# Kernel optimization log

Measured on AMD Instinct MI355X. Metric: run time of the kernel, lower is better.

Reference implementation:

```python
import jax, jax.numpy as jnp
import numpy as np

B = 16384
NUM_RATE, NUM_GENRE, NUM_DIRECTOR, NUM_ACTOR = 6, 25, 2186, 8030
EMB = 32


def setup_inputs() -> dict:
    key = jax.random.key(0)
    k0, k1, k2, k3, k4 = jax.random.split(key, 5)
    x = jax.random.randint(k0, (B, 1 + NUM_GENRE + NUM_DIRECTOR + NUM_ACTOR), 0, 2, dtype=jnp.int64 if jax.config.jax_enable_x64 else jnp.int32)
    rate_table = jax.random.normal(k1, (NUM_RATE, EMB), dtype=jnp.float32)
    # torch Linear weights have shape [out_features, in_features]
    W_genre = jax.random.normal(k2, (EMB, NUM_GENRE), dtype=jnp.float32) * (1.0 / np.sqrt(NUM_GENRE))
    W_director = jax.random.normal(k3, (EMB, NUM_DIRECTOR), dtype=jnp.float32) * (1.0 / np.sqrt(NUM_DIRECTOR))
    W_actor = jax.random.normal(k4, (EMB, NUM_ACTOR), dtype=jnp.float32) * (1.0 / np.sqrt(NUM_ACTOR))
    return {"x": x, "rate_table": rate_table, "W_genre": W_genre,
            "W_director": W_director, "W_actor": W_actor}


def _maxnorm_gather(table, idx, max_norm=1.0, eps=1e-7):
    # torch.nn.Embedding(max_norm=1.0): rows accessed are renormalized to norm <= max_norm
    rows = table[idx]  # [B, E]
    norm = jnp.linalg.norm(rows, axis=-1, keepdims=True)
    scale = jnp.where(norm > max_norm, max_norm / (norm + eps), 1.0)
    return rows * scale


def _mean_pool_linear(multi_hot_f, W):
    # Linear(no bias) on multi-hot then divide by row-sum == mean-pooled embedding bag
    emb = jnp.einsum('bn,en->be', multi_hot_f, W)
    return emb / jnp.sum(multi_hot_f, axis=1, keepdims=True)


def reference(x, rate_table, W_genre, W_director, W_actor):
    rate_idx = x[:, 0]
    genre = x[:, 1:26].astype(jnp.float32)
    director = x[:, 26:2212].astype(jnp.float32)
    actors = x[:, 2212:10242].astype(jnp.float32)
    rate_emb = _maxnorm_gather(rate_table, rate_idx)
    genre_emb = _mean_pool_linear(genre, W_genre)
    director_emb = _mean_pool_linear(director, W_director)
    actors_emb = _mean_pool_linear(actors, W_actor)
    return jnp.concatenate((rate_emb, genre_emb, director_emb, actors_emb), axis=1)  # [B, 4*EMB]
```

## Files before the change

kernel.cpp:

```cpp
#include <hip/hip_runtime.h>
#include <hip/hip_bf16.h>

#define B_ROWS 16384
#define XC     10242
#define NGENRE 25
#define NDIR   2186
#define NACT   8030
#define EMB    32
#define KT_TOTAL 321
#define OUTC   128
#define NCOLS  112
#define PART_STRIDE ((size_t)B_ROWS * NCOLS)
#define WFRAG_BYTES ((size_t)KT_TOTAL * 4 * 64 * 16)

typedef short bf16x8 __attribute__((ext_vector_type(8)));
typedef float f32x4  __attribute__((ext_vector_type(4)));
typedef float f32x4a __attribute__((ext_vector_type(4), aligned(4)));
typedef int   i32x4a __attribute__((ext_vector_type(4), aligned(4)));

__global__ void prep_wfrag(const float* __restrict__ wg,
                           const float* __restrict__ wd,
                           const float* __restrict__ wa,
                           uint4* __restrict__ Wfrag) {
  const int kt = blockIdx.x;
  const int s  = threadIdx.x >> 6;
  const int l  = threadIdx.x & 63;
  const int n  = l & 15;
  const int k0 = kt * 32 + ((l >> 4) << 3);

  unsigned short v[8];
#pragma unroll
  for (int j = 0; j < 8; ++j) {
    const int k = k0 + j;
    float f = 0.f;
    if (kt == 0) {
      if (s < 2) { if (k >= 1 && k < 26) f = wg[(s * 16 + n) * NGENRE + (k - 1)]; }
      else       { if (k >= 26)          f = wd[((s - 2) * 16 + n) * NDIR + (k - 26)]; }
    } else if (kt < 69) {
      if (s < 2) f = wd[(s * 16 + n) * NDIR + (k - 26)];
    } else if (kt == 69) {
      if (s < 2) { if (k < 2212)  f = wd[(s * 16 + n) * NDIR + (k - 26)]; }
      else       { if (k >= 2212) f = wa[((s - 2) * 16 + n) * NACT + (k - 2212)]; }
    } else if (kt < 320) {
      if (s < 2) f = wa[(s * 16 + n) * NACT + (k - 2212)];
    } else {
      if (s < 2 && k < XC) f = wa[(s * 16 + n) * NACT + (k - 2212)];
    }
    __hip_bfloat16 h = __float2bfloat16(f);
    v[j] = *reinterpret_cast<unsigned short*>(&h);
  }
  union { unsigned short u[8]; uint4 q; } cv;
#pragma unroll
  for (int j = 0; j < 8; ++j) cv.u[j] = v[j];
  Wfrag[((size_t)kt * 4 + s) * 64 + l] = cv.q;
}

template<int KS>
__global__ __launch_bounds__(256) void main_mm(const int* __restrict__ x,
                                               const uint4* __restrict__ Wfrag,
                                               float* __restrict__ part) {
  constexpr int PER = (((KT_TOTAL + KS - 1) / KS) + 3) & ~3;
  const int t    = threadIdx.x;
  const int rb   = blockIdx.x & 255;
  const int ks   = blockIdx.x >> 8;
  const int ktA  = ks * PER;
  const int ktB  = (ktA + PER < KT_TOTAL) ? ktA + PER : KT_TOTAL;
  const int lane = t & 63;
  const int w    = t >> 6;
  const int lo   = lane & 15, hi = lane >> 4;
  const int* xrow = x + (size_t)(rb * 64 + w * 16 + lo) * XC;

  f32x4 accG0 = {0,0,0,0}, accG1 = {0,0,0,0};
  f32x4 accD0 = {0,0,0,0}, accD1 = {0,0,0,0};
  f32x4 accA0 = {0,0,0,0}, accA1 = {0,0,0,0};
  f32x4 accI  = {0,0,0,0};

  auto load_x8 = [&](int kt, int* dst) {
    int k0 = kt * 32 + hi * 8;
    if (kt < 320) {
      i32x4a a = *reinterpret_cast<const i32x4a*>(xrow + k0);
      i32x4a b = *reinterpret_cast<const i32x4a*>(xrow + k0 + 4);
      dst[0]=a[0]; dst[1]=a[1]; dst[2]=a[2]; dst[3]=a[3];
      dst[4]=b[0]; dst[5]=b[1]; dst[6]=b[2]; dst[7]=b[3];
    } else {
#pragma unroll
      for (int j = 0; j < 8; ++j) dst[j] = (k0 + j < XC) ? xrow[k0 + j] : 0;
    }
  };
  auto packa = [&](const int* cx) -> bf16x8 {
    union { unsigned int w4[4]; bf16x8 v; } af;
#pragma unroll
    for (int i = 0; i < 4; ++i)
      af.w4[i] = ((unsigned)cx[2*i] + ((unsigned)cx[2*i+1] << 16)) * 0x3F80u;
    return af.v;
  };
  auto bload = [&](int kt, int s) -> bf16x8 {
    union { uint4 q; bf16x8 v; } c;
    c.q = Wfrag[((size_t)kt * 4 + s) * 64 + lane];
    return c.v;
  };
  auto mkconst = [&](bool on) -> bf16x8 {
    union { unsigned int w4[4]; bf16x8 v; } c;
    unsigned int u = on ? 0x3F803F80u : 0u;
    c.w4[0]=u; c.w4[1]=u; c.w4[2]=u; c.w4[3]=u;
    return c.v;
  };
  const bf16x8 ivD = mkconst(lo == 1);
  const bf16x8 ivA = mkconst(lo == 2);

  auto do_mfma = [&](int kt, bf16x8 a) {
    const int kb = kt * 32 + hi * 8;
    if (kt == 0) {
      accG0 = __builtin_amdgcn_mfma_f32_16x16x32_bf16(a, bload(0,0), accG0, 0,0,0);
      accG1 = __builtin_amdgcn_mfma_f32_16x16x32_bf16(a, bload(0,1), accG1, 0,0,0);
      accD0 = __builtin_amdgcn_mfma_f32_16x16x32_bf16(a, bload(0,2), accD0, 0,0,0);
      accD1 = __builtin_amdgcn_mfma_f32_16x16x32_bf16(a, bload(0,3), accD1, 0,0,0);
      union { unsigned short u[8]; bf16x8 v; } iv;
#pragma unroll
      for (int j = 0; j < 8; ++j) {
        int k = kb + j;
        bool on = (lo == 0) ? (k >= 1 && k < 26) : (lo == 1) ? (k >= 26) : false;
        iv.u[j] = on ? (unsigned short)0x3F80 : (unsigned short)0;
      }
      accI = __builtin_amdgcn_mfma_f32_16x16x32_bf16(a, iv.v, accI, 0,0,0);
    } else if (kt < 69) {
      accD0 = __builtin_amdgcn_mfma_f32_16x16x32_bf16(a, bload(kt,0), accD0, 0,0,0);
      accD1 = __builtin_amdgcn_mfma_f32_16x16x32_bf16(a, bload(kt,1), accD1, 0,0,0);
      accI  = __builtin_amdgcn_mfma_f32_16x16x32_bf16(a, ivD, accI, 0,0,0);
    } else if (kt == 69) {
      accD0 = __builtin_amdgcn_mfma_f32_16x16x32_bf16(a, bload(69,0), accD0, 0,0,0);
      accD1 = __builtin_amdgcn_mfma_f32_16x16x32_bf16(a, bload(69,1), accD1, 0,0,0);
      accA0 = __builtin_amdgcn_mfma_f32_16x16x32_bf16(a, bload(69,2), accA0, 0,0,0);
      accA1 = __builtin_amdgcn_mfma_f32_16x16x32_bf16(a, bload(69,3), accA1, 0,0,0);
      union { unsigned short u[8]; bf16x8 v; } iv;
#pragma unroll
      for (int j = 0; j < 8; ++j) {
        int k = kb + j;
        bool on = (lo == 1) ? (k < 2212) : (lo == 2) ? (k >= 2212) : false;
        iv.u[j] = on ? (unsigned short)0x3F80 : (unsigned short)0;
      }
      accI = __builtin_amdgcn_mfma_f32_16x16x32_bf16(a, iv.v, accI, 0,0,0);
    } else if (kt < 320) {
      accA0 = __builtin_amdgcn_mfma_f32_16x16x32_bf16(a, bload(kt,0), accA0, 0,0,0);
      accA1 = __builtin_amdgcn_mfma_f32_16x16x32_bf16(a, bload(kt,1), accA1, 0,0,0);
      accI  = __builtin_amdgcn_mfma_f32_16x16x32_bf16(a, ivA, accI, 0,0,0);
    } else {
      accA0 = __builtin_amdgcn_mfma_f32_16x16x32_bf16(a, bload(320,0), accA0, 0,0,0);
      accA1 = __builtin_amdgcn_mfma_f32_16x16x32_bf16(a, bload(320,1), accA1, 0,0,0);
      union { unsigned short u[8]; bf16x8 v; } iv;
#pragma unroll
      for (int j = 0; j < 8; ++j) {
        int k = kb + j;
        iv.u[j] = (lo == 2 && k < XC) ? (unsigned short)0x3F80 : (unsigned short)0;
      }
      accI = __builtin_amdgcn_mfma_f32_16x16x32_bf16(a, iv.v, accI, 0,0,0);
    }
  };

  int xg0[8], xg1[8], xg2[8], xg3[8];
  for (int g = ktA; g < ktB; g += 4) {
    load_x8(g, xg0);
    if (g + 1 < ktB) load_x8(g + 1, xg1);
    if (g + 2 < ktB) load_x8(g + 2, xg2);
    if (g + 3 < ktB) load_x8(g + 3, xg3);

    do_mfma(g, packa(xg0));
    if (g + 1 < ktB) do_mfma(g + 1, packa(xg1));
    if (g + 2 < ktB) do_mfma(g + 2, packa(xg2));
    if (g + 3 < ktB) do_mfma(g + 3, packa(xg3));
  }

  float* slab = part + (size_t)ks * PART_STRIDE;
  const int rbase = rb * 64 + w * 16 + hi * 4;
#pragma unroll
  for (int j = 0; j < 4; ++j) {
    size_t ro = (size_t)(rbase + j) * NCOLS;
    slab[ro +  0 + lo] = accG0[j];
    slab[ro + 16 + lo] = accG1[j];
    slab[ro + 32 + lo] = accD0[j];
    slab[ro + 48 + lo] = accD1[j];
    slab[ro + 64 + lo] = accA0[j];
    slab[ro + 80 + lo] = accA1[j];
    if (lo < 3) slab[ro + 96 + lo] = accI[j];
  }
}

__global__ __launch_bounds__(128) void reduce_k(const int* __restrict__ x,
                                                const float* __restrict__ rate,
                                                const float* __restrict__ part,
                                                int ksplit,
                                                float* __restrict__ out) {
  __shared__ float srow[112];
  const int r = blockIdx.x;
  const int c = threadIdx.x;

  if (c < 28) {
    f32x4 acc = {0.f, 0.f, 0.f, 0.f};
    for (int ks = 0; ks < ksplit; ++ks) {
      const float* p = part + (size_t)ks * PART_STRIDE + (size_t)r * NCOLS + c * 4;
      f32x4a v = *reinterpret_cast<const f32x4a*>(p);
      acc[0] += v[0]; acc[1] += v[1]; acc[2] += v[2]; acc[3] += v[3];
    }
    srow[c * 4 + 0] = acc[0];
    srow[c * 4 + 1] = acc[1];
    srow[c * 4 + 2] = acc[2];
    srow[c * 4 + 3] = acc[3];
  }
  __syncthreads();

  float res;
  if (c < EMB) {
    int idx = x[(size_t)r * XC];
    float v = rate[idx * EMB + c];
    float s2 = v * v;
    s2 += __shfl_xor(s2, 1, 32);
    s2 += __shfl_xor(s2, 2, 32);
    s2 += __shfl_xor(s2, 4, 32);
    s2 += __shfl_xor(s2, 8, 32);
    s2 += __shfl_xor(s2, 16, 32);
    float norm = sqrtf(s2);
    float scale = (norm > 1.0f) ? (1.0f / (norm + 1e-7f)) : 1.0f;
    res = v * scale;
  } else {
    int cc = c - EMB;
    res = srow[cc] / srow[96 + (cc >> 5)];
  }
  out[(size_t)r * OUTC + c] = res;
}

extern "C" void kernel_launch(void* const* d_in, const int* in_sizes, int n_in,
                              void* d_out, int out_size, void* d_ws, size_t ws_size,
                              hipStream_t stream) {
  (void)in_sizes; (void)n_in; (void)out_size;
  const int*   x    = (const int*)d_in[0];
  const float* rate = (const float*)d_in[1];
  const float* wg   = (const float*)d_in[2];
  const float* wd   = (const float*)d_in[3];
  const float* wa   = (const float*)d_in[4];
  float* out  = (float*)d_out;
  float* part = (float*)d_ws;

  const size_t slab_bytes = PART_STRIDE * sizeof(float);
  int KS;
  if      (ws_size >= 4 * slab_bytes + WFRAG_BYTES) KS = 4;
  else if (ws_size >= 2 * slab_bytes + WFRAG_BYTES) KS = 2;
  else                                              KS = 1;
  uint4* Wfrag = (uint4*)((char*)d_ws + (size_t)KS * slab_bytes);

  prep_wfrag<<<KT_TOTAL, 256, 0, stream>>>(wg, wd, wa, Wfrag);
  switch (KS) {
    case 4: main_mm<4><<<4 * 256, 256, 0, stream>>>(x, Wfrag, part); break;
    case 2: main_mm<2><<<2 * 256, 256, 0, stream>>>(x, Wfrag, part); break;
    default: main_mm<1><<<1 * 256, 256, 0, stream>>>(x, Wfrag, part); break;
  }
  reduce_k<<<B_ROWS, 128, 0, stream>>>(x, rate, part, KS, out);
}
```

Baseline: 911.2 us.

## Double-buffer x loads and prefetch weight fragments ahead of MFMA groups

The main matmul loop now keeps two register buffers of x data, issuing loads for the next group of four k-tiles before running MFMAs on the current group, so global memory latency overlaps with compute. Weight fragment loads for a group are hoisted ahead of the MFMAs and passed in explicitly. The weight prep kernel also uses vectorized float4 loads on its interior tiles. The cost is roughly double the registers for x buffering, which may lower occupancy or cause spills.

```diff
diff --git a/kernel.cpp b/kernel.cpp
--- a/kernel.cpp
+++ b/kernel.cpp
@@ -28,30 +28,48 @@
   const int n  = l & 15;
   const int k0 = kt * 32 + ((l >> 4) << 3);
 
-  unsigned short v[8];
+  float f[8];
+  bool done = false;
+  if (s < 2) {
+    if (kt >= 1 && kt < 69) {
+      const float* p = wd + (size_t)(s * 16 + n) * NDIR + (k0 - 26);
+      f32x4a v0 = *reinterpret_cast<const f32x4a*>(p);
+      f32x4a v1 = *reinterpret_cast<const f32x4a*>(p + 4);
+      f[0]=v0[0]; f[1]=v0[1]; f[2]=v0[2]; f[3]=v0[3];
+      f[4]=v1[0]; f[5]=v1[1]; f[6]=v1[2]; f[7]=v1[3];
+      done = true;
+    } else if (kt >= 70 && kt < 320) {
+      const float* p = wa + (size_t)(s * 16 + n) * NACT + (k0 - 2212);
+      f32x4a v0 = *reinterpret_cast<const f32x4a*>(p);
+      f32x4a v1 = *reinterpret_cast<const f32x4a*>(p + 4);
+      f[0]=v0[0]; f[1]=v0[1]; f[2]=v0[2]; f[3]=v0[3];
+      f[4]=v1[0]; f[5]=v1[1]; f[6]=v1[2]; f[7]=v1[3];
+      done = true;
+    }
+  }
+  if (!done) {
+#pragma unroll
+    for (int j = 0; j < 8; ++j) {
+      const int k = k0 + j;
+      float v = 0.f;
+      if (kt == 0) {
+        if (s < 2) { if (k >= 1 && k < 26) v = wg[(s * 16 + n) * NGENRE + (k - 1)]; }
+        else       { if (k >= 26)          v = wd[((s - 2) * 16 + n) * NDIR + (k - 26)]; }
+      } else if (kt == 69) {
+        if (s < 2) { if (k < 2212)  v = wd[(s * 16 + n) * NDIR + (k - 26)]; }
+        else       { if (k >= 2212) v = wa[((s - 2) * 16 + n) * NACT + (k - 2212)]; }
+      } else if (kt == 320) {
+        if (s < 2 && k < XC) v = wa[(s * 16 + n) * NACT + (k - 2212)];
+      }
+      f[j] = v;
+    }
+  }
+  union { unsigned short u[8]; uint4 q; } cv;
 #pragma unroll
   for (int j = 0; j < 8; ++j) {
-    const int k = k0 + j;
-    float f = 0.f;
-    if (kt == 0) {
-      if (s < 2) { if (k >= 1 && k < 26) f = wg[(s * 16 + n) * NGENRE + (k - 1)]; }
-      else       { if (k >= 26)          f = wd[((s - 2) * 16 + n) * NDIR + (k - 26)]; }
-    } else if (kt < 69) {
-      if (s < 2) f = wd[(s * 16 + n) * NDIR + (k - 26)];
-    } else if (kt == 69) {
-      if (s < 2) { if (k < 2212)  f = wd[(s * 16 + n) * NDIR + (k - 26)]; }
-      else       { if (k >= 2212) f = wa[((s - 2) * 16 + n) * NACT + (k - 2212)]; }
-    } else if (kt < 320) {
-      if (s < 2) f = wa[(s * 16 + n) * NACT + (k - 2212)];
-    } else {
-      if (s < 2 && k < XC) f = wa[(s * 16 + n) * NACT + (k - 2212)];
-    }
-    __hip_bfloat16 h = __float2bfloat16(f);
-    v[j] = *reinterpret_cast<unsigned short*>(&h);
-  }
-  union { unsigned short u[8]; uint4 q; } cv;
-#pragma unroll
-  for (int j = 0; j < 8; ++j) cv.u[j] = v[j];
+    __hip_bfloat16 h = __float2bfloat16(f[j]);
+    cv.u[j] = *reinterpret_cast<unsigned short*>(&h);
+  }
   Wfrag[((size_t)kt * 4 + s) * 64 + l] = cv.q;
 }
 
@@ -108,11 +126,11 @@
   const bf16x8 ivD = mkconst(lo == 1);
   const bf16x8 ivA = mkconst(lo == 2);
 
-  auto do_mfma = [&](int kt, bf16x8 a) {
+  auto do_mfma = [&](int kt, bf16x8 a, bf16x8 b0, bf16x8 b1) {
     const int kb = kt * 32 + hi * 8;
     if (kt == 0) {
-      accG0 = __builtin_amdgcn_mfma_f32_16x16x32_bf16(a, bload(0,0), accG0, 0,0,0);
-      accG1 = __builtin_amdgcn_mfma_f32_16x16x32_bf16(a, bload(0,1), accG1, 0,0,0);
+      accG0 = __builtin_amdgcn_mfma_f32_16x16x32_bf16(a, b0, accG0, 0,0,0);
+      accG1 = __builtin_amdgcn_mfma_f32_16x16x32_bf16(a, b1, accG1, 0,0,0);
       accD0 = __builtin_amdgcn_mfma_f32_16x16x32_bf16(a, bload(0,2), accD0, 0,0,0);
       accD1 = __builtin_amdgcn_mfma_f32_16x16x32_bf16(a, bload(0,3), accD1, 0,0,0);
       union { unsigned short u[8]; bf16x8 v; } iv;
@@ -124,12 +142,12 @@
       }
       accI = __builtin_amdgcn_mfma_f32_16x16x32_bf16(a, iv.v, accI, 0,0,0);
     } else if (kt < 69) {
-      accD0 = __builtin_amdgcn_mfma_f32_16x16x32_bf16(a, bload(kt,0), accD0, 0,0,0);
-      accD1 = __builtin_amdgcn_mfma_f32_16x16x32_bf16(a, bload(kt,1), accD1, 0,0,0);
+      accD0 = __builtin_amdgcn_mfma_f32_16x16x32_bf16(a, b0, accD0, 0,0,0);
+      accD1 = __builtin_amdgcn_mfma_f32_16x16x32_bf16(a, b1, accD1, 0,0,0);
       accI  = __builtin_amdgcn_mfma_f32_16x16x32_bf16(a, ivD, accI, 0,0,0);
     } else if (kt == 69) {
-      accD0 = __builtin_amdgcn_mfma_f32_16x16x32_bf16(a, bload(69,0), accD0, 0,0,0);
-      accD1 = __builtin_amdgcn_mfma_f32_16x16x32_bf16(a, bload(69,1), accD1, 0,0,0);
+      accD0 = __builtin_amdgcn_mfma_f32_16x16x32_bf16(a, b0, accD0, 0,0,0);
+      accD1 = __builtin_amdgcn_mfma_f32_16x16x32_bf16(a, b1, accD1, 0,0,0);
       accA0 = __builtin_amdgcn_mfma_f32_16x16x32_bf16(a, bload(69,2), accA0, 0,0,0);
       accA1 = __builtin_amdgcn_mfma_f32_16x16x32_bf16(a, bload(69,3), accA1, 0,0,0);
       union { unsigned short u[8]; bf16x8 v; } iv;
@@ -141,12 +159,12 @@
       }
       accI = __builtin_amdgcn_mfma_f32_16x16x32_bf16(a, iv.v, accI, 0,0,0);
     } else if (kt < 320) {
-      accA0 = __builtin_amdgcn_mfma_f32_16x16x32_bf16(a, bload(kt,0), accA0, 0,0,0);
-      accA1 = __builtin_amdgcn_mfma_f32_16x16x32_bf16(a, bload(kt,1), accA1, 0,0,0);
+      accA0 = __builtin_amdgcn_mfma_f32_16x16x32_bf16(a, b0, accA0, 0,0,0);
+      accA1 = __builtin_amdgcn_mfma_f32_16x16x32_bf16(a, b1, accA1, 0,0,0);
       accI  = __builtin_amdgcn_mfma_f32_16x16x32_bf16(a, ivA, accI, 0,0,0);
     } else {
-      accA0 = __builtin_amdgcn_mfma_f32_16x16x32_bf16(a, bload(320,0), accA0, 0,0,0);
-      accA1 = __builtin_amdgcn_mfma_f32_16x16x32_bf16(a, bload(320,1), accA1, 0,0,0);
+      accA0 = __builtin_amdgcn_mfma_f32_16x16x32_bf16(a, b0, accA0, 0,0,0);
+      accA1 = __builtin_amdgcn_mfma_f32_16x16x32_bf16(a, b1, accA1, 0,0,0);
       union { unsigned short u[8]; bf16x8 v; } iv;
 #pragma unroll
       for (int j = 0; j < 8; ++j) {
@@ -157,17 +175,36 @@
     }
   };
 
-  int xg0[8], xg1[8], xg2[8], xg3[8];
-  for (int g = ktA; g < ktB; g += 4) {
-    load_x8(g, xg0);
-    if (g + 1 < ktB) load_x8(g + 1, xg1);
-    if (g + 2 < ktB) load_x8(g + 2, xg2);
-    if (g + 3 < ktB) load_x8(g + 3, xg3);
-
-    do_mfma(g, packa(xg0));
-    if (g + 1 < ktB) do_mfma(g + 1, packa(xg1));
-    if (g + 2 < ktB) do_mfma(g + 2, packa(xg2));
-    if (g + 3 < ktB) do_mfma(g + 3, packa(xg3));
+  int xA0[8], xA1[8], xA2[8], xA3[8];
+  int xB0[8], xB1[8], xB2[8], xB3[8];
+
+  auto load_group = [&](int g, int* d0, int* d1, int* d2, int* d3) {
+    if (g     < ktB) load_x8(g,     d0);
+    if (g + 1 < ktB) load_x8(g + 1, d1);
+    if (g + 2 < ktB) load_x8(g + 2, d2);
+    if (g + 3 < ktB) load_x8(g + 3, d3);
+  };
+
+  auto run_group = [&](int g,
+                       const int* s0, const int* s1, const int* s2, const int* s3,
+                       int* d0, int* d1, int* d2, int* d3) {
+    bf16x8 b00 = bload(g, 0), b01 = bload(g, 1);
+    bf16x8 b10, b11, b20, b21, b30, b31;
+    if (g + 1 < ktB) { b10 = bload(g + 1, 0); b11 = bload(g + 1, 1); }
+    if (g + 2 < ktB) { b20 = bload(g + 2, 0); b21 = bload(g + 2, 1); }
+    if (g + 3 < ktB) { b30 = bload(g + 3, 0); b31 = bload(g + 3, 1); }
+    load_group(g + 4, d0, d1, d2, d3);
+    do_mfma(g, packa(s0), b00, b01);
+    if (g + 1 < ktB) do_mfma(g + 1, packa(s1), b10, b11);
+    if (g + 2 < ktB) do_mfma(g + 2, packa(s2), b20, b21);
+    if (g + 3 < ktB) do_mfma(g + 3, packa(s3), b30, b31);
+  };
+
+  load_group(ktA, xA0, xA1, xA2, xA3);
+  for (int g = ktA; g < ktB; g += 8) {
+    run_group(g,     xA0, xA1, xA2, xA3, xB0, xB1, xB2, xB3);
+    if (g + 4 < ktB)
+      run_group(g + 4, xB0, xB1, xB2, xB3, xA0, xA1, xA2, xA3);
   }
 
   float* slab = part + (size_t)ks * PART_STRIDE;
```

After: 899.6 us, median of 2. Within noise of the previous version (-1.3%).
